# Kernel optimization log

Hardware: AMD Instinct MI355X
Metric: run time of the kernel (lower is better)

## Reference

```python
import jax, jax.numpy as jnp
import numpy as np

D_MODEL = 1024
NUM_HEADS = 16
D_HEAD = D_MODEL // NUM_HEADS
B, S = 2, 2048


def setup_inputs() -> dict:
    key = jax.random.key(0)
    ks = jax.random.split(key, 12)
    s = 0.02
    return {
        "query": jax.random.normal(ks[0], (B, S, D_MODEL), jnp.float32),
        "key": jax.random.normal(ks[1], (B, S, D_MODEL), jnp.float32),
        "value": jax.random.normal(ks[2], (B, S, D_MODEL), jnp.float32),
        "mask": jnp.ones((B, 1, 1, S), jnp.float32),
        "W_q": jax.random.normal(ks[3], (D_MODEL, D_MODEL), jnp.float32) * s,
        "b_q": jnp.zeros((D_MODEL,), jnp.float32),
        "W_k": jax.random.normal(ks[4], (D_MODEL, D_MODEL), jnp.float32) * s,
        "b_k": jnp.zeros((D_MODEL,), jnp.float32),
        "W_v": jax.random.normal(ks[5], (D_MODEL, D_MODEL), jnp.float32) * s,
        "b_v": jnp.zeros((D_MODEL,), jnp.float32),
        "W_o": jax.random.normal(ks[6], (D_MODEL, D_MODEL), jnp.float32) * s,
        "b_o": jnp.zeros((D_MODEL,), jnp.float32),
    }


def reference(query, key, value, mask, W_q, b_q, W_k, b_k, W_v, b_v, W_o, b_o):
    # Linear projections (torch nn.Linear: x @ W.T + b; here W stored as [in, out])
    q = query @ W_q + b_q
    k = key @ W_k + b_k
    v = value @ W_v + b_v
    # [B, S, D] -> [B, H, S, Dh]
    def split_heads(x):
        b, s, _ = x.shape
        return x.reshape(b, s, NUM_HEADS, D_HEAD).transpose(0, 2, 1, 3)
    q, k, v = split_heads(q), split_heads(k), split_heads(v)
    # scaled dot-product attention; full [B,H,Sq,Sk] matrix (faithful to source)
    logits = jnp.einsum("bhqd,bhkd->bhqk", q, k) / jnp.sqrt(jnp.float32(D_HEAD))
    logits = logits + (1.0 - mask) * (-1e9)
    attn = jax.nn.softmax(logits, axis=-1)
    # dropout is identity in eval mode
    ctx = jnp.einsum("bhqk,bhkd->bhqd", attn, v)
    ctx = ctx.transpose(0, 2, 1, 3).reshape(ctx.shape[0], -1, D_MODEL)
    out = ctx @ W_o + b_o
    return out, attn
```

## Files before the change

kernel.cpp:

```cpp
#include <hip/hip_runtime.h>
#include <hip/hip_bf16.h>

#define BATCH 2
#define SEQ 2048
#define DM 1024
#define NH 16
#define DH 64
#define MTOT (BATCH*SEQ)

typedef __attribute__((ext_vector_type(8))) short bf16x8;
typedef __attribute__((ext_vector_type(4))) float f32x4;
typedef __attribute__((ext_vector_type(16))) float f32x16;
typedef __attribute__((ext_vector_type(4))) float float4v;
typedef __attribute__((ext_vector_type(8))) unsigned short u16x8;
typedef __attribute__((ext_vector_type(4))) unsigned short u16x4;

#define GLDS16(g, l) __builtin_amdgcn_global_load_lds(                         \
    (const __attribute__((address_space(1))) void*)(g),                        \
    (__attribute__((address_space(3))) void*)(l), 16, 0, 0)

static __device__ __forceinline__ float bf2f(unsigned short u) {
    unsigned int x = ((unsigned int)u) << 16;
    float f; __builtin_memcpy(&f, &x, 4); return f;
}
static __device__ __forceinline__ unsigned short f2bf(float f) {
    unsigned int x; __builtin_memcpy(&x, &f, 4);
    x += 0x7fffu + ((x >> 16) & 1);
    return (unsigned short)(x >> 16);
}
static __device__ __forceinline__ unsigned int cvt_pk_bf16(float a, float b) {
    unsigned int r;
    asm volatile("v_cvt_pk_bf16_f32 %0, %1, %2" : "=v"(r) : "v"(a), "v"(b));
    return r;
}

__global__ __launch_bounds__(256) void prep_kernel(
    const float* __restrict__ q, const float* __restrict__ k, const float* __restrict__ v,
    unsigned short* __restrict__ oq, unsigned short* __restrict__ ok_, unsigned short* __restrict__ ov,
    const float* __restrict__ w0, const float* __restrict__ w1,
    const float* __restrict__ w2, const float* __restrict__ w3,
    unsigned short* __restrict__ t0, unsigned short* __restrict__ t1,
    unsigned short* __restrict__ t2, unsigned short* __restrict__ t3) {
    __shared__ float tile[64][65];
    const int bx = blockIdx.x, t = threadIdx.x;
    if (bx < 6144) {
        const int slab = bx >> 11, bxr = bx & 2047;
        const float* in = slab == 0 ? q : (slab == 1 ? k : v);
        unsigned short* out = slab == 0 ? oq : (slab == 1 ? ok_ : ov);
        size_t i = ((size_t)bxr * 256 + t) * 8;
        float4v a = *(const float4v*)(in + i);
        float4v b = *(const float4v*)(in + i + 4);
        u16x8 r;
        r[0]=f2bf(a[0]); r[1]=f2bf(a[1]); r[2]=f2bf(a[2]); r[3]=f2bf(a[3]);
        r[4]=f2bf(b[0]); r[5]=f2bf(b[1]); r[6]=f2bf(b[2]); r[7]=f2bf(b[3]);
        *(u16x8*)(out + i) = r;
    } else {
        const int i2 = bx - 6144;
        const int z = i2 >> 8, rem = i2 & 255;
        const float* w = z==0 ? w0 : z==1 ? w1 : z==2 ? w2 : w3;
        unsigned short* wt = z==0 ? t0 : z==1 ? t1 : z==2 ? t2 : t3;
        const int k0 = (rem & 15) * 64, n0 = (rem >> 4) * 64;
        const int tr = t >> 4, tc = t & 15;
#pragma unroll
        for (int i = 0; i < 4; ++i) {
            float4v val = *(const float4v*)(w + (size_t)(k0 + tr + 16*i) * DM + n0 + tc*4);
            tile[tr + 16*i][tc*4 + 0] = val[0];
            tile[tr + 16*i][tc*4 + 1] = val[1];
            tile[tr + 16*i][tc*4 + 2] = val[2];
            tile[tr + 16*i][tc*4 + 3] = val[3];
        }
        __syncthreads();
#pragma unroll
        for (int i = 0; i < 4; ++i) {
            u16x4 o;
#pragma unroll
            for (int j = 0; j < 4; ++j) o[j] = f2bf(tile[tc*4 + j][tr + 16*i]);
            *(u16x4*)(wt + (size_t)(n0 + tr + 16*i) * DM + k0 + tc*4) = o;
        }
    }
}

template<int OUTMODE>
static __device__ __forceinline__ void gemm_body(
    const unsigned short* __restrict__ A, const unsigned short* __restrict__ Bt,
    const float* __restrict__ bias, void* __restrict__ Cout,
    unsigned short* a_lds, unsigned short* b_lds) {
    constexpr int BM = 128, BN = 128, BK = 64, NT = DM / BK;
    const int tid = threadIdx.x;
    const int m0 = blockIdx.y * BM, n0 = blockIdx.x * BN;
    const int w = tid >> 6, l = tid & 63;
    const int lr = l & 15, lg = l >> 4;
    const int wm = (w >> 1) * 64, wn = (w & 1) * 64;
    f32x4 acc[4][4] = {};

    auto stage = [&](int buf, int kt) {
        const int k0 = kt * BK;
#pragma unroll
        for (int i = 0; i < 4; ++i) {
            int u = i*256 + tid;
            int row = u >> 3, slot = u & 7;
            int sc = (slot ^ (row & 7)) * 8;
            GLDS16(A + (size_t)(m0 + row)*DM + k0 + sc, a_lds + buf*BM*BK + u*8);
        }
#pragma unroll
        for (int i = 0; i < 4; ++i) {
            int u = i*256 + tid;
            int row = u >> 3, slot = u & 7;
            int sc = (slot ^ (row & 7)) * 8;
            GLDS16(Bt + (size_t)(n0 + row)*DM + k0 + sc, b_lds + buf*BN*BK + u*8);
        }
    };

    stage(0, 0);
    for (int kt = 0; kt < NT; ++kt) {
        __syncthreads();
        if (kt < NT-1) stage((kt+1)&1, kt+1);
        const char* ab = (const char*)(a_lds + (kt&1)*BM*BK);
        const char* bb = (const char*)(b_lds + (kt&1)*BN*BK);
        bf16x8 af[4][2], bfr[4][2];
#pragma unroll
        for (int r = 0; r < 4; ++r)
#pragma unroll
            for (int kc = 0; kc < 2; ++kc) {
                int row = wm + r*16 + lr;
                af[r][kc] = *(const bf16x8*)(ab + row*128 + ((kc*64 + lg*16) ^ ((row&7)<<4)));
            }
#pragma unroll
        for (int c = 0; c < 4; ++c)
#pragma unroll
            for (int kc = 0; kc < 2; ++kc) {
                int row = wn + c*16 + lr;
                bfr[c][kc] = *(const bf16x8*)(bb + row*128 + ((kc*64 + lg*16) ^ ((row&7)<<4)));
            }
#pragma unroll
        for (int r = 0; r < 4; ++r)
#pragma unroll
            for (int c = 0; c < 4; ++c)
#pragma unroll
                for (int kc = 0; kc < 2; ++kc)
                    acc[r][c] = __builtin_amdgcn_mfma_f32_16x16x32_bf16(af[r][kc], bfr[c][kc], acc[r][c], 0, 0, 0);
    }

#pragma unroll
    for (int r = 0; r < 4; ++r)
#pragma unroll
        for (int c = 0; c < 4; ++c) {
            int m = m0 + wm + r*16 + lg*4;
            int n = n0 + wn + c*16 + lr;
            float bb = bias[n];
            if constexpr (OUTMODE == 1) {
                float* o = (float*)Cout;
#pragma unroll
                for (int j = 0; j < 4; ++j) o[(size_t)(m+j)*DM + n] = acc[r][c][j] + bb;
            } else if constexpr (OUTMODE == 0) {
                unsigned short* o = (unsigned short*)Cout;
#pragma unroll
                for (int j = 0; j < 4; ++j) o[(size_t)(m+j)*DM + n] = f2bf(acc[r][c][j] + bb);
            } else {
                unsigned short* o = (unsigned short*)Cout;
                int bb_ = m >> 11, kk = m & (SEQ-1);
                int bh = bb_ * NH + (n >> 6), d = n & 63;
                u16x4 ov;
#pragma unroll
                for (int j = 0; j < 4; ++j) ov[j] = f2bf(acc[r][c][j] + bb);
                *(u16x4*)(o + ((size_t)bh*DH + d)*SEQ + kk) = ov;
            }
        }
}

__global__ __launch_bounds__(256) void gemm_qkv_kernel(
    const unsigned short* __restrict__ A0, const unsigned short* __restrict__ A1, const unsigned short* __restrict__ A2,
    const unsigned short* __restrict__ B0, const unsigned short* __restrict__ B1, const unsigned short* __restrict__ B2,
    const float* __restrict__ c0, const float* __restrict__ c1, const float* __restrict__ c2,
    unsigned short* __restrict__ O0, unsigned short* __restrict__ O1, unsigned short* __restrict__ O2) {
    __shared__ __align__(16) unsigned short smem[2*128*64 + 2*128*64];
    const int z = blockIdx.z;
    const unsigned short* A = z==0 ? A0 : z==1 ? A1 : A2;
    const unsigned short* B = z==0 ? B0 : z==1 ? B1 : B2;
    const float* c = z==0 ? c0 : z==1 ? c1 : c2;
    unsigned short* O = z==0 ? O0 : z==1 ? O1 : O2;
    if (z == 2) gemm_body<2>(A, B, c, O, smem, smem + 2*128*64);
    else        gemm_body<0>(A, B, c, O, smem, smem + 2*128*64);
}

__global__ __launch_bounds__(256) void gemm_out_kernel(
    const unsigned short* __restrict__ A, const unsigned short* __restrict__ Bt,
    const float* __restrict__ bias, float* __restrict__ Cout) {
    __shared__ __align__(16) unsigned short smem[2*128*64 + 2*128*64];
    gemm_body<1>(A, Bt, bias, Cout, smem, smem + 2*128*64);
}

__global__ __launch_bounds__(512) void attn_kernel(
    const unsigned short* __restrict__ qw, const unsigned short* __restrict__ kw,
    const unsigned short* __restrict__ vtg, const float* __restrict__ mask,
    float* __restrict__ attn_out, unsigned short* __restrict__ ctx) {
    constexpr int QB = 128, KB = 64, NT2 = SEQ / KB / 2;
    __shared__ __align__(16) unsigned short smem[2*2*KB*DH + 2*2*KB*DH];
    unsigned short* kbuf = smem;
    unsigned short* vbuf = smem + 4*KB*DH;
    const int tid = threadIdx.x, w = tid >> 6, l = tid & 63;
    const int hh = w >> 2, ws = w & 3;
    const int q32 = l & 31, hi = l >> 5;
    const int u0 = (blockIdx.x & 7) * 64 + (blockIdx.x >> 3);
    const int qblk = u0 & 15, bh = u0 >> 4;
    const int b = bh >> 4, h = bh & 15;
    const int q0 = qblk * QB;
    const int q = q0 + ws*32 + q32;
    const int kbase = hh * (SEQ/2);

    bf16x8 qf[4];
    {
        const unsigned short* qp = qw + ((size_t)(b*SEQ + q))*DM + h*DH + hi*8;
#pragma unroll
        for (int ks = 0; ks < 4; ++ks) {
            bf16x8 t = *(const bf16x8*)(qp + ks*16);
#pragma unroll
            for (int j = 0; j < 8; ++j) t[j] = (short)f2bf(bf2f((unsigned short)t[j]) * 0.125f);
            qf[ks] = t;
        }
    }

    auto stageK = [&](int buf, int kt) {
#pragma unroll
        for (int hf = 0; hf < 2; ++hf) {
            int row = tid >> 3, slot = tid & 7;
            int sc = (slot ^ (row & 7)) * 8;
            const unsigned short* base = kw + ((size_t)(b*SEQ + hf*(SEQ/2) + kt*KB + row))*DM + h*DH;
            GLDS16(base + sc, kbuf + (buf*2 + hf)*KB*DH + tid*8);
        }
    };
    auto stageV = [&](int buf, int kt) {
#pragma unroll
        for (int hf = 0; hf < 2; ++hf) {
            int row = tid >> 3, slot = tid & 7;
            int sc = (slot ^ (row & 7)) * 8;
            const unsigned short* base = vtg + ((size_t)bh*DH + row)*SEQ + hf*(SEQ/2) + kt*KB;
            GLDS16(base + sc, vbuf + (buf*2 + hf)*KB*DH + tid*8);
        }
    };

    const float* mrow = mask + (size_t)b*SEQ + kbase;

    float rs = 0.f;
    stageK(0, 0);
    for (int kt = 0; kt < NT2; ++kt) {
        __syncthreads();
        if (kt < NT2-1) stageK((kt+1)&1, kt+1);
        const char* kb = (const char*)(kbuf + ((kt&1)*2 + hh)*KB*DH);
#pragma unroll
        for (int sub = 0; sub < 2; ++sub) {
            f32x16 s = {};
#pragma unroll
            for (int ks = 0; ks < 4; ++ks) {
                int key = sub*32 + q32;
                bf16x8 kf = *(const bf16x8*)(kb + key*128 + ((ks*32 + hi*16) ^ ((key&7)<<4)));
                s = __builtin_amdgcn_mfma_f32_32x32x16_bf16(kf, qf[ks], s, 0, 0, 0);
            }
#pragma unroll
            for (int rq = 0; rq < 4; ++rq) {
                float4v m4 = *(const float4v*)(mrow + kt*KB + sub*32 + rq*8 + hi*4);
#pragma unroll
                for (int r = 0; r < 4; ++r)
                    rs += __expf(s[rq*4 + r] + (1.0f - m4[r]) * (-1e9f));
            }
        }
    }
    rs += __shfl_xor(rs, 32);
    {
        float* rbuf = (float*)smem;
        __syncthreads();
        rbuf[w*64 + l] = rs;
        __syncthreads();
        rs += rbuf[(w ^ 4)*64 + l];
        __syncthreads();
    }
    const float rinv = 1.0f / rs;

    f32x16 oacc[2] = {};
    float* attn_row = attn_out + ((size_t)bh*SEQ + q)*SEQ + kbase;
    stageK(0, 0); stageV(0, 0);
    for (int kt = 0; kt < NT2; ++kt) {
        __syncthreads();
        if (kt < NT2-1) { stageK((kt+1)&1, kt+1); stageV((kt+1)&1, kt+1); }
        const char* kb = (const char*)(kbuf + ((kt&1)*2 + hh)*KB*DH);
        const char* vb = (const char*)(vbuf + ((kt&1)*2 + hh)*KB*DH);
#pragma unroll
        for (int sub = 0; sub < 2; ++sub) {
            f32x16 s = {};
#pragma unroll
            for (int ks = 0; ks < 4; ++ks) {
                int key = sub*32 + q32;
                bf16x8 kf = *(const bf16x8*)(kb + key*128 + ((ks*32 + hi*16) ^ ((key&7)<<4)));
                s = __builtin_amdgcn_mfma_f32_32x32x16_bf16(kf, qf[ks], s, 0, 0, 0);
            }
            float p[16];
#pragma unroll
            for (int rq = 0; rq < 4; ++rq) {
                float4v m4 = *(const float4v*)(mrow + kt*KB + sub*32 + rq*8 + hi*4);
                float4v pv;
#pragma unroll
                for (int r = 0; r < 4; ++r) {
                    pv[r] = __expf(s[rq*4 + r] + (1.0f - m4[r]) * (-1e9f)) * rinv;
                    p[rq*4 + r] = pv[r];
                }
                *(float4v*)(attn_row + kt*KB + sub*32 + rq*8 + hi*4) = pv;
            }
#pragma unroll
            for (int half = 0; half < 2; ++half) {
                unsigned int w0 = cvt_pk_bf16(p[half*8+0], p[half*8+1]);
                unsigned int w1 = cvt_pk_bf16(p[half*8+2], p[half*8+3]);
                unsigned int w2 = cvt_pk_bf16(p[half*8+4], p[half*8+5]);
                unsigned int w3 = cvt_pk_bf16(p[half*8+6], p[half*8+7]);
                asm volatile("v_permlane32_swap_b32 %0, %1" : "+v"(w0), "+v"(w2));
                asm volatile("v_permlane32_swap_b32 %0, %1" : "+v"(w1), "+v"(w3));
                union { unsigned int uu[4]; bf16x8 v; } pa;
                pa.uu[0] = w0; pa.uu[1] = w1; pa.uu[2] = w2; pa.uu[3] = w3;
                const int ks4 = sub*2 + half;
#pragma unroll
                for (int dsub = 0; dsub < 2; ++dsub) {
                    int d = dsub*32 + q32;
                    bf16x8 vf = *(const bf16x8*)(vb + d*128 + ((ks4*32 + hi*16) ^ ((d&7)<<4)));
                    oacc[dsub] = __builtin_amdgcn_mfma_f32_32x32x16_bf16(pa.v, vf, oacc[dsub], 0, 0, 0);
                }
            }
        }
    }

    float* cbuf = (float*)smem;
    __syncthreads();
    if (w >= 4) {
        int base = ((w - 4)*64 + l) * 36;
        *(f32x16*)(cbuf + base) = oacc[0];
        *(f32x16*)(cbuf + base + 16) = oacc[1];
    }
    __syncthreads();
    if (w < 4) {
        int base = (w*64 + l) * 36;
        oacc[0] += *(const f32x16*)(cbuf + base);
        oacc[1] += *(const f32x16*)(cbuf + base + 16);
#pragma unroll
        for (int dsub = 0; dsub < 2; ++dsub) {
            int d = h*DH + dsub*32 + q32;
#pragma unroll
            for (int reg = 0; reg < 16; ++reg) {
                int qr = q0 + ws*32 + (reg&3) + 8*(reg>>2) + 4*hi;
                ctx[(size_t)(b*SEQ + qr)*DM + d] = f2bf(oacc[dsub][reg]);
            }
        }
    }
}

extern "C" void kernel_launch(void* const* d_in, const int* in_sizes, int n_in,
                              void* d_out, int out_size, void* d_ws, size_t ws_size,
                              hipStream_t stream) {
    const float* query = (const float*)d_in[0];
    const float* key_  = (const float*)d_in[1];
    const float* value = (const float*)d_in[2];
    const float* mask  = (const float*)d_in[3];
    const float* W_q = (const float*)d_in[4];
    const float* b_q = (const float*)d_in[5];
    const float* W_k = (const float*)d_in[6];
    const float* b_k = (const float*)d_in[7];
    const float* W_v = (const float*)d_in[8];
    const float* b_v = (const float*)d_in[9];
    const float* W_o = (const float*)d_in[10];
    const float* b_o = (const float*)d_in[11];

    char* ws = (char*)d_ws;
    const size_t SZ = (size_t)MTOT * DM * 2;
    unsigned short* xq  = (unsigned short*)(ws);
    unsigned short* xk  = (unsigned short*)(ws + SZ);
    unsigned short* xv  = (unsigned short*)(ws + 2*SZ);
    unsigned short* wtq = (unsigned short*)(ws + 3*SZ);
    unsigned short* wtk = wtq + (size_t)DM*DM;
    unsigned short* wtv = wtk + (size_t)DM*DM;
    unsigned short* wto = wtv + (size_t)DM*DM;
    unsigned short* qws = (unsigned short*)(ws + 4*SZ);
    unsigned short* kws = (unsigned short*)(ws + 5*SZ);
    unsigned short* vtg = (unsigned short*)(ws + 6*SZ);
    unsigned short* ctx = (unsigned short*)(ws + 7*SZ);
    float* out_f  = (float*)d_out;
    float* attn_f = out_f + (size_t)MTOT * DM;

    prep_kernel<<<dim3(7168), 256, 0, stream>>>(query, key_, value, xq, xk, xv,
                                                W_q, W_k, W_v, W_o, wtq, wtk, wtv, wto);
    gemm_qkv_kernel<<<dim3(8, 32, 3), 256, 0, stream>>>(xq, xk, xv, wtq, wtk, wtv,
                                                        b_q, b_k, b_v, qws, kws, vtg);
    attn_kernel<<<dim3(512), 512, 0, stream>>>(qws, kws, vtg, mask, attn_f, ctx);
    gemm_out_kernel<<<dim3(8, 32), 256, 0, stream>>>(ctx, wto, b_o, out_f);
}
```

Measured before the change: 292.9 us.

## Drop LDS staging and key-split in attention; halve output GEMM N tile

The attention kernel no longer splits the key range across two half-blocks with LDS-staged K/V double buffering. Each of four waves now walks all keys and reads K and V^T fragments straight from global memory. This removes the cross-wave reductions, barriers and LDS use, but every wave reloads K/V through the cache and loses the swizzled LDS reuse. Separately, the output projection GEMM is templated to BN=64, doubling its grid to 512 blocks so more CUs are busy.

```diff
diff --git a/kernel.cpp b/kernel.cpp
--- a/kernel.cpp
+++ b/kernel.cpp
@@ -80,18 +80,18 @@
     }
 }
 
-template<int OUTMODE>
+template<int OUTMODE, int BN>
 static __device__ __forceinline__ void gemm_body(
     const unsigned short* __restrict__ A, const unsigned short* __restrict__ Bt,
     const float* __restrict__ bias, void* __restrict__ Cout,
     unsigned short* a_lds, unsigned short* b_lds) {
-    constexpr int BM = 128, BN = 128, BK = 64, NT = DM / BK;
+    constexpr int BM = 128, BK = 64, NT = DM / BK, NC = BN / 32;
     const int tid = threadIdx.x;
     const int m0 = blockIdx.y * BM, n0 = blockIdx.x * BN;
     const int w = tid >> 6, l = tid & 63;
     const int lr = l & 15, lg = l >> 4;
-    const int wm = (w >> 1) * 64, wn = (w & 1) * 64;
-    f32x4 acc[4][4] = {};
+    const int wm = (w >> 1) * 64, wn = (w & 1) * (BN/2);
+    f32x4 acc[4][NC] = {};
 
     auto stage = [&](int buf, int kt) {
         const int k0 = kt * BK;
@@ -103,7 +103,7 @@
             GLDS16(A + (size_t)(m0 + row)*DM + k0 + sc, a_lds + buf*BM*BK + u*8);
         }
 #pragma unroll
-        for (int i = 0; i < 4; ++i) {
+        for (int i = 0; i < NC; ++i) {
             int u = i*256 + tid;
             int row = u >> 3, slot = u & 7;
             int sc = (slot ^ (row & 7)) * 8;
@@ -117,7 +117,7 @@
         if (kt < NT-1) stage((kt+1)&1, kt+1);
         const char* ab = (const char*)(a_lds + (kt&1)*BM*BK);
         const char* bb = (const char*)(b_lds + (kt&1)*BN*BK);
-        bf16x8 af[4][2], bfr[4][2];
+        bf16x8 af[4][2], bfr[NC][2];
 #pragma unroll
         for (int r = 0; r < 4; ++r)
 #pragma unroll
@@ -126,7 +126,7 @@
                 af[r][kc] = *(const bf16x8*)(ab + row*128 + ((kc*64 + lg*16) ^ ((row&7)<<4)));
             }
 #pragma unroll
-        for (int c = 0; c < 4; ++c)
+        for (int c = 0; c < NC; ++c)
 #pragma unroll
             for (int kc = 0; kc < 2; ++kc) {
                 int row = wn + c*16 + lr;
@@ -135,7 +135,7 @@
 #pragma unroll
         for (int r = 0; r < 4; ++r)
 #pragma unroll
-            for (int c = 0; c < 4; ++c)
+            for (int c = 0; c < NC; ++c)
 #pragma unroll
                 for (int kc = 0; kc < 2; ++kc)
                     acc[r][c] = __builtin_amdgcn_mfma_f32_16x16x32_bf16(af[r][kc], bfr[c][kc], acc[r][c], 0, 0, 0);
@@ -144,7 +144,7 @@
 #pragma unroll
     for (int r = 0; r < 4; ++r)
 #pragma unroll
-        for (int c = 0; c < 4; ++c) {
+        for (int c = 0; c < NC; ++c) {
             int m = m0 + wm + r*16 + lg*4;
             int n = n0 + wn + c*16 + lr;
             float bb = bias[n];
@@ -179,34 +179,29 @@
     const unsigned short* B = z==0 ? B0 : z==1 ? B1 : B2;
     const float* c = z==0 ? c0 : z==1 ? c1 : c2;
     unsigned short* O = z==0 ? O0 : z==1 ? O1 : O2;
-    if (z == 2) gemm_body<2>(A, B, c, O, smem, smem + 2*128*64);
-    else        gemm_body<0>(A, B, c, O, smem, smem + 2*128*64);
+    if (z == 2) gemm_body<2, 128>(A, B, c, O, smem, smem + 2*128*64);
+    else        gemm_body<0, 128>(A, B, c, O, smem, smem + 2*128*64);
 }
 
 __global__ __launch_bounds__(256) void gemm_out_kernel(
     const unsigned short* __restrict__ A, const unsigned short* __restrict__ Bt,
     const float* __restrict__ bias, float* __restrict__ Cout) {
-    __shared__ __align__(16) unsigned short smem[2*128*64 + 2*128*64];
-    gemm_body<1>(A, Bt, bias, Cout, smem, smem + 2*128*64);
-}
-
-__global__ __launch_bounds__(512) void attn_kernel(
+    __shared__ __align__(16) unsigned short smem[2*128*64 + 2*64*64];
+    gemm_body<1, 64>(A, Bt, bias, Cout, smem, smem + 2*128*64);
+}
+
+__global__ __launch_bounds__(256, 3) void attn_kernel(
     const unsigned short* __restrict__ qw, const unsigned short* __restrict__ kw,
     const unsigned short* __restrict__ vtg, const float* __restrict__ mask,
     float* __restrict__ attn_out, unsigned short* __restrict__ ctx) {
-    constexpr int QB = 128, KB = 64, NT2 = SEQ / KB / 2;
-    __shared__ __align__(16) unsigned short smem[2*2*KB*DH + 2*2*KB*DH];
-    unsigned short* kbuf = smem;
-    unsigned short* vbuf = smem + 4*KB*DH;
+    constexpr int QB = 128, KB = 64, NT = SEQ / KB;
     const int tid = threadIdx.x, w = tid >> 6, l = tid & 63;
-    const int hh = w >> 2, ws = w & 3;
     const int q32 = l & 31, hi = l >> 5;
     const int u0 = (blockIdx.x & 7) * 64 + (blockIdx.x >> 3);
     const int qblk = u0 & 15, bh = u0 >> 4;
     const int b = bh >> 4, h = bh & 15;
     const int q0 = qblk * QB;
-    const int q = q0 + ws*32 + q32;
-    const int kbase = hh * (SEQ/2);
+    const int q = q0 + w*32 + q32;
 
     bf16x8 qf[4];
     {
@@ -220,42 +215,19 @@
         }
     }
 
-    auto stageK = [&](int buf, int kt) {
-#pragma unroll
-        for (int hf = 0; hf < 2; ++hf) {
-            int row = tid >> 3, slot = tid & 7;
-            int sc = (slot ^ (row & 7)) * 8;
-            const unsigned short* base = kw + ((size_t)(b*SEQ + hf*(SEQ/2) + kt*KB + row))*DM + h*DH;
-            GLDS16(base + sc, kbuf + (buf*2 + hf)*KB*DH + tid*8);
-        }
-    };
-    auto stageV = [&](int buf, int kt) {
-#pragma unroll
-        for (int hf = 0; hf < 2; ++hf) {
-            int row = tid >> 3, slot = tid & 7;
-            int sc = (slot ^ (row & 7)) * 8;
-            const unsigned short* base = vtg + ((size_t)bh*DH + row)*SEQ + hf*(SEQ/2) + kt*KB;
-            GLDS16(base + sc, vbuf + (buf*2 + hf)*KB*DH + tid*8);
-        }
-    };
-
-    const float* mrow = mask + (size_t)b*SEQ + kbase;
+    const unsigned short* kb0 = kw + ((size_t)(b*SEQ) + q32)*DM + h*DH + hi*8;
+    const unsigned short* vb0 = vtg + ((size_t)bh*DH + q32)*SEQ + hi*8;
+    const float* mrow = mask + (size_t)b*SEQ;
 
     float rs = 0.f;
-    stageK(0, 0);
-    for (int kt = 0; kt < NT2; ++kt) {
-        __syncthreads();
-        if (kt < NT2-1) stageK((kt+1)&1, kt+1);
-        const char* kb = (const char*)(kbuf + ((kt&1)*2 + hh)*KB*DH);
+    for (int kt = 0; kt < NT; ++kt) {
 #pragma unroll
         for (int sub = 0; sub < 2; ++sub) {
+            const unsigned short* kp = kb0 + (size_t)(kt*KB + sub*32)*DM;
             f32x16 s = {};
 #pragma unroll
-            for (int ks = 0; ks < 4; ++ks) {
-                int key = sub*32 + q32;
-                bf16x8 kf = *(const bf16x8*)(kb + key*128 + ((ks*32 + hi*16) ^ ((key&7)<<4)));
-                s = __builtin_amdgcn_mfma_f32_32x32x16_bf16(kf, qf[ks], s, 0, 0, 0);
-            }
+            for (int ks = 0; ks < 4; ++ks)
+                s = __builtin_amdgcn_mfma_f32_32x32x16_bf16(*(const bf16x8*)(kp + ks*16), qf[ks], s, 0, 0, 0);
 #pragma unroll
             for (int rq = 0; rq < 4; ++rq) {
                 float4v m4 = *(const float4v*)(mrow + kt*KB + sub*32 + rq*8 + hi*4);
@@ -266,33 +238,19 @@
         }
     }
     rs += __shfl_xor(rs, 32);
-    {
-        float* rbuf = (float*)smem;
-        __syncthreads();
-        rbuf[w*64 + l] = rs;
-        __syncthreads();
-        rs += rbuf[(w ^ 4)*64 + l];
-        __syncthreads();
-    }
     const float rinv = 1.0f / rs;
 
     f32x16 oacc[2] = {};
-    float* attn_row = attn_out + ((size_t)bh*SEQ + q)*SEQ + kbase;
-    stageK(0, 0); stageV(0, 0);
-    for (int kt = 0; kt < NT2; ++kt) {
-        __syncthreads();
-        if (kt < NT2-1) { stageK((kt+1)&1, kt+1); stageV((kt+1)&1, kt+1); }
-        const char* kb = (const char*)(kbuf + ((kt&1)*2 + hh)*KB*DH);
-        const char* vb = (const char*)(vbuf + ((kt&1)*2 + hh)*KB*DH);
+    float* attn_row = attn_out + ((size_t)bh*SEQ + q)*SEQ;
+    for (int kt = 0; kt < NT; ++kt) {
+        const unsigned short* vp = vb0 + kt*KB;
 #pragma unroll
         for (int sub = 0; sub < 2; ++sub) {
+            const unsigned short* kp = kb0 + (size_t)(kt*KB + sub*32)*DM;
             f32x16 s = {};
 #pragma unroll
-            for (int ks = 0; ks < 4; ++ks) {
-                int key = sub*32 + q32;
-                bf16x8 kf = *(const bf16x8*)(kb + key*128 + ((ks*32 + hi*16) ^ ((key&7)<<4)));
-                s = __builtin_amdgcn_mfma_f32_32x32x16_bf16(kf, qf[ks], s, 0, 0, 0);
-            }
+            for (int ks = 0; ks < 4; ++ks)
+                s = __builtin_amdgcn_mfma_f32_32x32x16_bf16(*(const bf16x8*)(kp + ks*16), qf[ks], s, 0, 0, 0);
             float p[16];
 #pragma unroll
             for (int rq = 0; rq < 4; ++rq) {
@@ -318,34 +276,19 @@
                 const int ks4 = sub*2 + half;
 #pragma unroll
                 for (int dsub = 0; dsub < 2; ++dsub) {
-                    int d = dsub*32 + q32;
-                    bf16x8 vf = *(const bf16x8*)(vb + d*128 + ((ks4*32 + hi*16) ^ ((d&7)<<4)));
+                    bf16x8 vf = *(const bf16x8*)(vp + (size_t)dsub*32*SEQ + ks4*16);
                     oacc[dsub] = __builtin_amdgcn_mfma_f32_32x32x16_bf16(pa.v, vf, oacc[dsub], 0, 0, 0);
                 }
             }
         }
     }
-
-    float* cbuf = (float*)smem;
-    __syncthreads();
-    if (w >= 4) {
-        int base = ((w - 4)*64 + l) * 36;
-        *(f32x16*)(cbuf + base) = oacc[0];
-        *(f32x16*)(cbuf + base + 16) = oacc[1];
-    }
-    __syncthreads();
-    if (w < 4) {
-        int base = (w*64 + l) * 36;
-        oacc[0] += *(const f32x16*)(cbuf + base);
-        oacc[1] += *(const f32x16*)(cbuf + base + 16);
-#pragma unroll
-        for (int dsub = 0; dsub < 2; ++dsub) {
-            int d = h*DH + dsub*32 + q32;
-#pragma unroll
-            for (int reg = 0; reg < 16; ++reg) {
-                int qr = q0 + ws*32 + (reg&3) + 8*(reg>>2) + 4*hi;
-                ctx[(size_t)(b*SEQ + qr)*DM + d] = f2bf(oacc[dsub][reg]);
-            }
+#pragma unroll
+    for (int dsub = 0; dsub < 2; ++dsub) {
+        int d = h*DH + dsub*32 + q32;
+#pragma unroll
+        for (int reg = 0; reg < 16; ++reg) {
+            int qr = q0 + w*32 + (reg&3) + 8*(reg>>2) + 4*hi;
+            ctx[(size_t)(b*SEQ + qr)*DM + d] = f2bf(oacc[dsub][reg]);
         }
     }
 }
@@ -386,6 +329,6 @@
                                                 W_q, W_k, W_v, W_o, wtq, wtk, wtv, wto);
     gemm_qkv_kernel<<<dim3(8, 32, 3), 256, 0, stream>>>(xq, xk, xv, wtq, wtk, wtv,
                                                         b_q, b_k, b_v, qws, kws, vtg);
-    attn_kernel<<<dim3(512), 512, 0, stream>>>(qws, kws, vtg, mask, attn_f, ctx);
-    gemm_out_kernel<<<dim3(8, 32), 256, 0, stream>>>(ctx, wto, b_o, out_f);
-}
+    attn_kernel<<<dim3(512), 256, 0, stream>>>(qws, kws, vtg, mask, attn_f, ctx);
+    gemm_out_kernel<<<dim3(16, 32), 256, 0, stream>>>(ctx, wto, b_o, out_f);
+}
```

New measurement: 403.2 us. +37.7%, slower.
